# Performance work log

Hardware: AMD Instinct MI355X
Metric: run time of the kernel (lower is better)

The kernel has to match this reference:

```python
import jax, jax.numpy as jnp
import numpy as np

IN_FEATURES = 512
HIDDEN = 512


def setup_inputs() -> dict:
    key = jax.random.key(0)
    ks = jax.random.split(key, 7)
    s = 1.0 / np.sqrt(IN_FEATURES)
    return {
        "x": jax.random.normal(ks[0], (8, 2048, IN_FEATURES), dtype=jnp.float32),
        "Wq": jax.random.uniform(ks[1], (IN_FEATURES, HIDDEN), jnp.float32, -s, s),
        "bq": jax.random.uniform(ks[2], (HIDDEN,), jnp.float32, -s, s),
        "Wk": jax.random.uniform(ks[3], (IN_FEATURES, HIDDEN), jnp.float32, -s, s),
        "bk": jax.random.uniform(ks[4], (HIDDEN,), jnp.float32, -s, s),
        "Wv": jax.random.uniform(ks[5], (IN_FEATURES, HIDDEN), jnp.float32, -s, s),
        "bv": jax.random.uniform(ks[6], (HIDDEN,), jnp.float32, -s, s),
    }


def reference(x, Wq, bq, Wk, bk, Wv, bv):
    # q,k,v: [b, s, h]
    q = jnp.einsum("bsf,fh->bsh", x, Wq) + bq
    k = jnp.einsum("bsf,fh->bsh", x, Wk) + bk
    v = jnp.einsum("bsf,fh->bsh", x, Wv) + bv
    # NOTE: no 1/sqrt(d) scaling, matching the original module.
    scores = jnp.einsum("bqh,bkh->bqk", q, k)  # [b, s, s]
    attn = jax.nn.softmax(scores, axis=-1)
    return jnp.einsum("bqk,bkh->bqh", attn, v)
```

## Files before the change

### kernel.cpp

```cpp
#include <hip/hip_runtime.h>
#include <hip/hip_fp16.h>


typedef _Float16 f16;
typedef __attribute__((ext_vector_type(8))) _Float16 f16x8;
typedef __attribute__((ext_vector_type(4))) _Float16 f16x4;
typedef __attribute__((ext_vector_type(4))) float f32x4;
typedef __attribute__((address_space(3))) char lds_t;

#define GADDR(p) ((const __attribute__((address_space(1))) void*)(p))
#define LADDR(p) ((__attribute__((address_space(3))) void*)(p))

__device__ __forceinline__ unsigned lds_u32(void* p) {
    return (unsigned)(unsigned long long)(lds_t*)p;
}

#define DSRD(dst, a) asm volatile("ds_read_b128 %0, %1" : "=v"(dst) : "v"(a))
#define WAITV0 asm volatile("s_waitcnt vmcnt(0)" ::: "memory")
#define WAITV8 asm volatile("s_waitcnt vmcnt(8)" ::: "memory")
#define WAITLG0 asm volatile("s_waitcnt lgkmcnt(0)" ::: "memory")

__device__ __forceinline__ void xcd_remap(int& bx, int& by, int& bz) {
    const int gx = gridDim.x, gy = gridDim.y;
    const int nwg = gx * gy * gridDim.z;
    const int f = (blockIdx.z * gy + blockIdx.y) * gx + blockIdx.x;
    int L = (f & 7) * (nwg >> 3) + (f >> 3);
    bx = L % gx; int r = L / gx; by = r % gy; bz = r / gy;
}

__global__ __launch_bounds__(256) void k_cvt_x(const float* __restrict__ in,
                                               f16* __restrict__ out) {
    long i = (long)blockIdx.x * 256 + threadIdx.x;
    float4 v = ((const float4*)in)[i];
    f16x4 h = { (f16)v.x, (f16)v.y, (f16)v.z, (f16)v.w };
    ((f16x4*)out)[i] = h;
}

__global__ __launch_bounds__(256) void k_cvt_w(const float* __restrict__ Wq,
                                               const float* __restrict__ Wk,
                                               const float* __restrict__ Wv,
                                               f16* __restrict__ Wt) {
    int id = blockIdx.x * 256 + threadIdx.x;
    int w = id >> 18, rem = id & 262143;
    int kk = rem >> 9, n = rem & 511;
    const float* W = (w == 0) ? Wq : (w == 1) ? Wk : Wv;
    Wt[((long)w << 18) + ((long)n << 9) + kk] = (f16)W[((long)kk << 9) + n];
}


#define G128STAGE(BUF, K0)                                                                  \
  { _Pragma("unroll") for (int i_ = 0; i_ < 4; ++i_) {                                      \
      const f16* sa_ = A + (rowA0 + i_ * 32 + (tid >> 3)) * (long)K + (K0) + colSw;         \
      __builtin_amdgcn_global_load_lds(GADDR(sa_),                                          \
          LADDR(smem + (BUF) * 32768 + i_ * 4096 + wave * 1024), 16, 0, 0);                 \
      const f16* sb_ = Bt + (rowB0 + i_ * 32 + (tid >> 3)) * (long)K + (K0) + colSw;        \
      __builtin_amdgcn_global_load_lds(GADDR(sb_),                                          \
          LADDR(smem + (BUF) * 32768 + 16384 + i_ * 4096 + wave * 1024), 16, 0, 0);         \
    } }

template <bool OUT_F16, bool QKV>
__global__ __launch_bounds__(256) void k_g128(const f16* __restrict__ Ain,
                                              const f16* __restrict__ Btin,
                                              void* __restrict__ Cv,
                                              void* __restrict__ CvAlt,
                                              const float* __restrict__ b0,
                                              const float* __restrict__ b1,
                                              const float* __restrict__ b2,
                                              int N, int K,
                                              long sA, long sB, long sC) {
    int bxi, byi, bz;
    xcd_remap(bxi, byi, bz);
    const f16* A  = Ain  + bz * sA;
    const f16* Bt = Btin + bz * sB;
    __shared__ __align__(16) char smem[65536];
    const unsigned sbase = lds_u32(smem);

    const int tid = threadIdx.x;
    const int wave = tid >> 6, lane = tid & 63;
    const int l15 = lane & 15, l4 = lane >> 4;
    const int wm = (wave >> 1) * 64, wn = (wave & 1) * 64;
    const long rowA0 = (long)byi * 128;
    const long rowB0 = (long)bxi * 128;

    const unsigned sw = (unsigned)((l15 & 7) << 4);
    const unsigned cb0 = (unsigned)(l4 * 16) ^ sw;
    const unsigned cb1 = (unsigned)(64 + l4 * 16) ^ sw;
    const int colSw = (((tid & 7) ^ ((tid >> 3) & 7)) << 3);

    f32x4 acc[4][4] = {};

    const int nt = K >> 6;
    G128STAGE(0, 0);
    int cur = 0;
    for (int t = 0; t < nt; ++t) {
        if (t + 1 < nt) { G128STAGE(cur ^ 1, (t + 1) << 6); WAITV8; }
        else            { WAITV0; }
        __builtin_amdgcn_s_barrier();

        f16x8 af[4][2], bf[4][2];
        const unsigned aB = sbase + (unsigned)cur * 32768u;
        const unsigned bB = aB + 16384u;
#pragma unroll
        for (int mi = 0; mi < 4; ++mi) {
            unsigned ra = wm + mi * 16 + l15;
            DSRD(af[mi][0], aB + ra * 128 + cb0);
            DSRD(af[mi][1], aB + ra * 128 + cb1);
        }
#pragma unroll
        for (int nj = 0; nj < 4; ++nj) {
            unsigned rb = wn + nj * 16 + l15;
            DSRD(bf[nj][0], bB + rb * 128 + cb0);
            DSRD(bf[nj][1], bB + rb * 128 + cb1);
        }
        WAITLG0;
        __builtin_amdgcn_sched_barrier(0);
        __builtin_amdgcn_s_setprio(1);
#pragma unroll
        for (int mi = 0; mi < 4; ++mi)
#pragma unroll
            for (int nj = 0; nj < 4; ++nj)
#pragma unroll
                for (int ks = 0; ks < 2; ++ks)
                    acc[mi][nj] = __builtin_amdgcn_mfma_f32_16x16x32_f16(
                        af[mi][ks], bf[nj][ks], acc[mi][nj], 0, 0, 0);
        __builtin_amdgcn_s_setprio(0);
        __builtin_amdgcn_s_barrier();
        cur ^= 1;
    }

    if constexpr (QKV) {
        if (bz == 2) {
            f16* VT = (f16*)CvAlt;
#pragma unroll
            for (int mi = 0; mi < 4; ++mi)
#pragma unroll
                for (int nj = 0; nj < 4; ++nj) {
                    long gr = rowA0 + wm + mi * 16 + l4 * 4;
                    int  gc = (int)rowB0 + wn + nj * 16 + l15;
                    float bv_ = b2[gc];
                    long b = gr >> 11, sL = gr & 2047;
                    f16x4 o = { (f16)(acc[mi][nj][0] + bv_),
                                (f16)(acc[mi][nj][1] + bv_),
                                (f16)(acc[mi][nj][2] + bv_),
                                (f16)(acc[mi][nj][3] + bv_) };
                    *(f16x4*)(VT + (b << 20) + ((long)gc << 11) + sL) = o;
                }
            return;
        }
    }

    const float* bias = nullptr;
    if constexpr (QKV) bias = (bz == 0) ? b0 : b1;

#pragma unroll
    for (int mi = 0; mi < 4; ++mi)
#pragma unroll
        for (int nj = 0; nj < 4; ++nj) {
            long gr = rowA0 + wm + mi * 16 + l4 * 4;
            int  gc = (int)rowB0 + wn + nj * 16 + l15;
            float bv_ = QKV ? bias[gc] : 0.f;
            if constexpr (OUT_F16) {
                f16* C = (f16*)Cv + bz * sC;
#pragma unroll
                for (int r = 0; r < 4; ++r)
                    C[(gr + r) * (long)N + gc] = (f16)(acc[mi][nj][r] + bv_);
            } else {
                float* C = (float*)Cv + bz * sC;
#pragma unroll
                for (int r = 0; r < 4; ++r)
                    C[(gr + r) * (long)N + gc] = acc[mi][nj][r] + bv_;
            }
        }
}

__global__ __launch_bounds__(256) void k_softmax(f16* __restrict__ P) {
    const long row = blockIdx.x;
    f16* p = P + row * 2048;
    const int tid = threadIdx.x, lane = tid & 63, wave = tid >> 6;

    f16x8 v = ((const f16x8*)p)[tid];
    float f[8];
#pragma unroll
    for (int j = 0; j < 8; ++j) f[j] = (float)v[j];
    float m = fmaxf(fmaxf(fmaxf(f[0], f[1]), fmaxf(f[2], f[3])),
                    fmaxf(fmaxf(f[4], f[5]), fmaxf(f[6], f[7])));
#pragma unroll
    for (int off = 32; off; off >>= 1) m = fmaxf(m, __shfl_xor(m, off));

    __shared__ float red[4];
    __shared__ float bc[2];
    if (lane == 0) red[wave] = m;
    __syncthreads();
    if (tid == 0) bc[0] = fmaxf(fmaxf(red[0], red[1]), fmaxf(red[2], red[3]));
    __syncthreads();
    m = bc[0];

    float e[8], sum = 0.f;
#pragma unroll
    for (int j = 0; j < 8; ++j) { e[j] = __expf(f[j] - m); sum += e[j]; }
#pragma unroll
    for (int off = 32; off; off >>= 1) sum += __shfl_xor(sum, off);
    if (lane == 0) red[wave] = sum;
    __syncthreads();
    if (tid == 0) bc[1] = (red[0] + red[1]) + (red[2] + red[3]);
    __syncthreads();
    float inv = 1.f / bc[1];

    f16x8 o;
#pragma unroll
    for (int j = 0; j < 8; ++j) o[j] = (f16)(e[j] * inv);
    ((f16x8*)p)[tid] = o;
}

extern "C" void kernel_launch(void* const* d_in, const int* in_sizes, int n_in,
                              void* d_out, int out_size, void* d_ws, size_t ws_size,
                              hipStream_t stream) {
    const float* x  = (const float*)d_in[0];
    const float* Wq = (const float*)d_in[1];
    const float* bq = (const float*)d_in[2];
    const float* Wk = (const float*)d_in[3];
    const float* bk = (const float*)d_in[4];
    const float* Wv = (const float*)d_in[5];
    const float* bv = (const float*)d_in[6];
    float* out = (float*)d_out;

    char* ws = (char*)d_ws;
    f16* vt = (f16*)(ws + 0);
    f16* xh = (f16*)(ws + 33554432);
    f16* Wt = (f16*)(ws + 50331648);
    f16* P8 = (f16*)(ws + 33554432);
    f16* qh = (f16*)d_out;
    f16* kh = (f16*)((char*)d_out + 16777216);

    k_cvt_x<<<8192, 256, 0, stream>>>(x, xh);
    k_cvt_w<<<3072, 256, 0, stream>>>(Wq, Wk, Wv, Wt);

    k_g128<true, true><<<dim3(4, 128, 3), 256, 0, stream>>>(
        xh, Wt, qh, vt, bq, bk, bv, 512, 512,
        0, (long)512 * 512, (long)16384 * 512);

    k_g128<true, false><<<dim3(16, 16, 8), 256, 0, stream>>>(
        qh, kh, P8, nullptr, nullptr, nullptr, nullptr, 2048, 512,
        (long)2048 * 512, (long)2048 * 512, (long)2048 * 2048);

    k_softmax<<<16384, 256, 0, stream>>>(P8);

    k_g128<false, false><<<dim3(4, 16, 8), 256, 0, stream>>>(
        P8, vt, out, nullptr, nullptr, nullptr, nullptr, 512, 2048,
        (long)2048 * 2048, (long)512 * 2048, (long)2048 * 512);
}
```

Measured before the change: 157.1 us.

## Chain multiple N-tiles per GEMM block and compile-time K with transposed score writes

The GEMM kernel now makes K a compile-time constant and adds a CHAIN parameter. Each workgroup walks several consecutive 128-wide B tiles in one continuous prefetch pipeline, reusing the same A rows and keeping the double-buffered loads flowing across tile boundaries. The QK^T GEMM swaps operands (K as A, Q as B) and writes transposed f16x4 vector stores instead of scalar stores. The goal is fewer workgroups, a shorter pipeline ramp per output tile, and wider stores. The cost is less grid parallelism (fewer blocks) and longer-running workgroups.

```diff
diff --git a/kernel.cpp b/kernel.cpp
--- a/kernel.cpp
+++ b/kernel.cpp
@@ -48,17 +48,17 @@
 }
 
 
-#define G128STAGE(BUF, K0)                                                                  \
+#define G128STAGE(BUF, RB, K0)                                                              \
   { _Pragma("unroll") for (int i_ = 0; i_ < 4; ++i_) {                                      \
       const f16* sa_ = A + (rowA0 + i_ * 32 + (tid >> 3)) * (long)K + (K0) + colSw;         \
       __builtin_amdgcn_global_load_lds(GADDR(sa_),                                          \
           LADDR(smem + (BUF) * 32768 + i_ * 4096 + wave * 1024), 16, 0, 0);                 \
-      const f16* sb_ = Bt + (rowB0 + i_ * 32 + (tid >> 3)) * (long)K + (K0) + colSw;        \
+      const f16* sb_ = Bt + ((RB) + i_ * 32 + (tid >> 3)) * (long)K + (K0) + colSw;         \
       __builtin_amdgcn_global_load_lds(GADDR(sb_),                                          \
           LADDR(smem + (BUF) * 32768 + 16384 + i_ * 4096 + wave * 1024), 16, 0, 0);         \
     } }
 
-template <bool OUT_F16, bool QKV>
+template <int MODE, int NT, int CHAIN>
 __global__ __launch_bounds__(256) void k_g128(const f16* __restrict__ Ain,
                                               const f16* __restrict__ Btin,
                                               void* __restrict__ Cv,
@@ -66,8 +66,12 @@
                                               const float* __restrict__ b0,
                                               const float* __restrict__ b1,
                                               const float* __restrict__ b2,
-                                              int N, int K,
+                                              int N,
                                               long sA, long sB, long sC) {
+    constexpr int K = NT << 6;
+    constexpr int LOGNT = (NT == 8) ? 3 : 5;
+    static_assert(NT == 8 || NT == 32, "NT");
+
     int bxi, byi, bz;
     xcd_remap(bxi, byi, bz);
     const f16* A  = Ain  + bz * sA;
@@ -80,7 +84,6 @@
     const int l15 = lane & 15, l4 = lane >> 4;
     const int wm = (wave >> 1) * 64, wn = (wave & 1) * 64;
     const long rowA0 = (long)byi * 128;
-    const long rowB0 = (long)bxi * 128;
 
     const unsigned sw = (unsigned)((l15 & 7) << 4);
     const unsigned cb0 = (unsigned)(l4 * 16) ^ sw;
@@ -89,88 +92,122 @@
 
     f32x4 acc[4][4] = {};
 
-    const int nt = K >> 6;
-    G128STAGE(0, 0);
+    G128STAGE(0, (long)bxi * CHAIN * 128, 0);
     int cur = 0;
-    for (int t = 0; t < nt; ++t) {
-        if (t + 1 < nt) { G128STAGE(cur ^ 1, (t + 1) << 6); WAITV8; }
-        else            { WAITV0; }
-        __builtin_amdgcn_s_barrier();
-
-        f16x8 af[4][2], bf[4][2];
-        const unsigned aB = sbase + (unsigned)cur * 32768u;
-        const unsigned bB = aB + 16384u;
-#pragma unroll
-        for (int mi = 0; mi < 4; ++mi) {
-            unsigned ra = wm + mi * 16 + l15;
-            DSRD(af[mi][0], aB + ra * 128 + cb0);
-            DSRD(af[mi][1], aB + ra * 128 + cb1);
+
+#pragma unroll 1
+    for (int c = 0; c < CHAIN; ++c) {
+#pragma unroll 1
+        for (int tt = 0; tt < NT; ++tt) {
+            const int un = c * NT + tt + 1;
+            if (un < NT * CHAIN) {
+                const long rBn = ((long)bxi * CHAIN + (un >> LOGNT)) * 128;
+                G128STAGE(cur ^ 1, rBn, (un & (NT - 1)) << 6);
+                WAITV8;
+            } else {
+                WAITV0;
+            }
+            __builtin_amdgcn_s_barrier();
+
+            f16x8 af[4][2], bf[4][2];
+            const unsigned aB = sbase + (unsigned)cur * 32768u;
+            const unsigned bB = aB + 16384u;
+#pragma unroll
+            for (int mi = 0; mi < 4; ++mi) {
+                unsigned ra = wm + mi * 16 + l15;
+                DSRD(af[mi][0], aB + ra * 128 + cb0);
+                DSRD(af[mi][1], aB + ra * 128 + cb1);
+            }
+#pragma unroll
+            for (int nj = 0; nj < 4; ++nj) {
+                unsigned rb = wn + nj * 16 + l15;
+                DSRD(bf[nj][0], bB + rb * 128 + cb0);
+                DSRD(bf[nj][1], bB + rb * 128 + cb1);
+            }
+            WAITLG0;
+            __builtin_amdgcn_sched_barrier(0);
+            __builtin_amdgcn_s_setprio(1);
+#pragma unroll
+            for (int mi = 0; mi < 4; ++mi)
+#pragma unroll
+                for (int nj = 0; nj < 4; ++nj)
+#pragma unroll
+                    for (int ks = 0; ks < 2; ++ks)
+                        acc[mi][nj] = __builtin_amdgcn_mfma_f32_16x16x32_f16(
+                            af[mi][ks], bf[nj][ks], acc[mi][nj], 0, 0, 0);
+            __builtin_amdgcn_s_setprio(0);
+            __builtin_amdgcn_s_barrier();
+            cur ^= 1;
         }
-#pragma unroll
-        for (int nj = 0; nj < 4; ++nj) {
-            unsigned rb = wn + nj * 16 + l15;
-            DSRD(bf[nj][0], bB + rb * 128 + cb0);
-            DSRD(bf[nj][1], bB + rb * 128 + cb1);
-        }
-        WAITLG0;
-        __builtin_amdgcn_sched_barrier(0);
-        __builtin_amdgcn_s_setprio(1);
-#pragma unroll
-        for (int mi = 0; mi < 4; ++mi)
-#pragma unroll
-            for (int nj = 0; nj < 4; ++nj)
-#pragma unroll
-                for (int ks = 0; ks < 2; ++ks)
-                    acc[mi][nj] = __builtin_amdgcn_mfma_f32_16x16x32_f16(
-                        af[mi][ks], bf[nj][ks], acc[mi][nj], 0, 0, 0);
-        __builtin_amdgcn_s_setprio(0);
-        __builtin_amdgcn_s_barrier();
-        cur ^= 1;
-    }
-
-    if constexpr (QKV) {
-        if (bz == 2) {
-            f16* VT = (f16*)CvAlt;
+
+        const long rowB0c = ((long)bxi * CHAIN + c) * 128;
+
+        if constexpr (MODE == 0) {
+            float* C = (float*)Cv + bz * sC;
 #pragma unroll
             for (int mi = 0; mi < 4; ++mi)
 #pragma unroll
                 for (int nj = 0; nj < 4; ++nj) {
                     long gr = rowA0 + wm + mi * 16 + l4 * 4;
-                    int  gc = (int)rowB0 + wn + nj * 16 + l15;
-                    float bv_ = b2[gc];
-                    long b = gr >> 11, sL = gr & 2047;
-                    f16x4 o = { (f16)(acc[mi][nj][0] + bv_),
-                                (f16)(acc[mi][nj][1] + bv_),
-                                (f16)(acc[mi][nj][2] + bv_),
-                                (f16)(acc[mi][nj][3] + bv_) };
-                    *(f16x4*)(VT + (b << 20) + ((long)gc << 11) + sL) = o;
+                    int  gc = (int)rowB0c + wn + nj * 16 + l15;
+#pragma unroll
+                    for (int r = 0; r < 4; ++r)
+                        C[(gr + r) * (long)N + gc] = acc[mi][nj][r];
                 }
-            return;
+        } else if constexpr (MODE == 1) {
+            if (bz == 2) {
+                f16* VT = (f16*)CvAlt;
+#pragma unroll
+                for (int mi = 0; mi < 4; ++mi)
+#pragma unroll
+                    for (int nj = 0; nj < 4; ++nj) {
+                        long gr = rowA0 + wm + mi * 16 + l4 * 4;
+                        int  gc = (int)rowB0c + wn + nj * 16 + l15;
+                        float bv_ = b2[gc];
+                        long b = gr >> 11, sL = gr & 2047;
+                        f16x4 o = { (f16)(acc[mi][nj][0] + bv_),
+                                    (f16)(acc[mi][nj][1] + bv_),
+                                    (f16)(acc[mi][nj][2] + bv_),
+                                    (f16)(acc[mi][nj][3] + bv_) };
+                        *(f16x4*)(VT + (b << 20) + ((long)gc << 11) + sL) = o;
+                    }
+            } else {
+                const float* bias = (bz == 0) ? b0 : b1;
+                f16* C = (f16*)Cv + bz * sC;
+#pragma unroll
+                for (int mi = 0; mi < 4; ++mi)
+#pragma unroll
+                    for (int nj = 0; nj < 4; ++nj) {
+                        long gr = rowA0 + wm + mi * 16 + l4 * 4;
+                        int  gc = (int)rowB0c + wn + nj * 16 + l15;
+                        float bv_ = bias[gc];
+#pragma unroll
+                        for (int r = 0; r < 4; ++r)
+                            C[(gr + r) * (long)N + gc] = (f16)(acc[mi][nj][r] + bv_);
+                    }
+            }
+        } else {
+            f16* C = (f16*)Cv + bz * sC;
+#pragma unroll
+            for (int mi = 0; mi < 4; ++mi)
+#pragma unroll
+                for (int nj = 0; nj < 4; ++nj) {
+                    long kb = rowA0 + wm + mi * 16 + l4 * 4;
+                    long q  = rowB0c + wn + nj * 16 + l15;
+                    f16x4 o = { (f16)acc[mi][nj][0], (f16)acc[mi][nj][1],
+                                (f16)acc[mi][nj][2], (f16)acc[mi][nj][3] };
+                    *(f16x4*)(C + q * (long)N + kb) = o;
+                }
+        }
+
+        if (c + 1 < CHAIN) {
+#pragma unroll
+            for (int mi = 0; mi < 4; ++mi)
+#pragma unroll
+                for (int nj = 0; nj < 4; ++nj)
+                    acc[mi][nj] = (f32x4){0.f, 0.f, 0.f, 0.f};
         }
     }
-
-    const float* bias = nullptr;
-    if constexpr (QKV) bias = (bz == 0) ? b0 : b1;
-
-#pragma unroll
-    for (int mi = 0; mi < 4; ++mi)
-#pragma unroll
-        for (int nj = 0; nj < 4; ++nj) {
-            long gr = rowA0 + wm + mi * 16 + l4 * 4;
-            int  gc = (int)rowB0 + wn + nj * 16 + l15;
-            float bv_ = QKV ? bias[gc] : 0.f;
-            if constexpr (OUT_F16) {
-                f16* C = (f16*)Cv + bz * sC;
-#pragma unroll
-                for (int r = 0; r < 4; ++r)
-                    C[(gr + r) * (long)N + gc] = (f16)(acc[mi][nj][r] + bv_);
-            } else {
-                float* C = (float*)Cv + bz * sC;
-#pragma unroll
-                for (int r = 0; r < 4; ++r)
-                    C[(gr + r) * (long)N + gc] = acc[mi][nj][r] + bv_;
-            }
-        }
 }
 
 __global__ __launch_bounds__(256) void k_softmax(f16* __restrict__ P) {
@@ -235,17 +272,17 @@
     k_cvt_x<<<8192, 256, 0, stream>>>(x, xh);
     k_cvt_w<<<3072, 256, 0, stream>>>(Wq, Wk, Wv, Wt);
 
-    k_g128<true, true><<<dim3(4, 128, 3), 256, 0, stream>>>(
-        xh, Wt, qh, vt, bq, bk, bv, 512, 512,
+    k_g128<1, 8, 2><<<dim3(2, 128, 3), 256, 0, stream>>>(
+        xh, Wt, qh, vt, bq, bk, bv, 512,
         0, (long)512 * 512, (long)16384 * 512);
 
-    k_g128<true, false><<<dim3(16, 16, 8), 256, 0, stream>>>(
-        qh, kh, P8, nullptr, nullptr, nullptr, nullptr, 2048, 512,
+    k_g128<2, 8, 4><<<dim3(4, 16, 8), 256, 0, stream>>>(
+        kh, qh, P8, nullptr, nullptr, nullptr, nullptr, 2048,
         (long)2048 * 512, (long)2048 * 512, (long)2048 * 2048);
 
     k_softmax<<<16384, 256, 0, stream>>>(P8);
 
-    k_g128<false, false><<<dim3(4, 16, 8), 256, 0, stream>>>(
-        P8, vt, out, nullptr, nullptr, nullptr, nullptr, 512, 2048,
+    k_g128<0, 32, 1><<<dim3(4, 16, 8), 256, 0, stream>>>(
+        P8, vt, out, nullptr, nullptr, nullptr, nullptr, 512,
         (long)2048 * 2048, (long)512 * 2048, (long)2048 * 512);
 }
```

Result: slower. 160.7 us (+2.3%).
